# Performance work log

Measured on AMD Instinct MI355X. Metric: run time of the kernel, lower is better.

The kernel has to match this reference:

```python
import jax, jax.numpy as jnp
import numpy as np

U = 50000
I = 25000
D = 128
NUM_INTERACTIONS = 800000
NUM_LAYERS = 3


def setup_inputs() -> dict:
    key = jax.random.key(0)
    k1, k2, k3, k4 = jax.random.split(key, 4)
    # LightGCN init: nn.init.normal_(emb.weight, std=1e-4)
    user_emb = jax.random.normal(k1, (U, D), dtype=jnp.float32) * 1e-4
    item_emb = jax.random.normal(k2, (I, D), dtype=jnp.float32) * 1e-4
    # Bipartite interactions; item node ids offset by U. Symmetric adjacency.
    u = jax.random.randint(k3, (NUM_INTERACTIONS,), 0, U, dtype=jnp.int32)
    it = jax.random.randint(k4, (NUM_INTERACTIONS,), U, U + I, dtype=jnp.int32)
    edge_src = jnp.concatenate([u, it])  # [E] destination rows of adj_t
    edge_dst = jnp.concatenate([it, u])  # [E] source cols (neighbors)
    return {"user_emb": user_emb, "item_emb": item_emb,
            "edge_src": edge_src, "edge_dst": edge_dst}


def reference(user_emb, item_emb, edge_src, edge_dst):
    N = U + I
    x = jnp.concatenate([user_emb, item_emb], axis=0)  # [N, D]
    # gcn_norm without self-loops: w_ij = deg_i^-1/2 * deg_j^-1/2
    ones = jnp.ones(edge_src.shape[0], dtype=x.dtype)
    deg = jax.ops.segment_sum(ones, edge_src, num_segments=N)
    dinv = jnp.where(deg > 0, jax.lax.rsqrt(jnp.maximum(deg, 1.0)), 0.0)
    w = dinv[edge_src] * dinv[edge_dst]  # [E]
    scale = 1.0 / (NUM_LAYERS + 1)
    avg = x * scale
    for _ in range(NUM_LAYERS):
        # SpMM: out[i] = sum_{j in N(i)} w_ij * x[j]
        x = jax.ops.segment_sum(w[:, None] * x[edge_dst], edge_src, num_segments=N)
        avg = avg + x * scale
    return avg[:U], avg[U:]
```

## Files before the change

### kernel.cpp

```cpp
#include <hip/hip_runtime.h>
#include <hip/hip_fp16.h>

#define U_N 50000
#define I_N 25000
#define D_N 128
#define N_N (U_N + I_N)

#define ROWS_PER_B 256
#define NBUCK 293
#define NBLK 256
#define SN (NBUCK * NBLK)

#define SCAN_ELEMS_PER_BLOCK 1024
#define NUM_SCAN_BLOCKS ((SN + SCAN_ELEMS_PER_BLOCK - 1) / SCAN_ELEMS_PER_BLOCK)
#define SN_PAD (NUM_SCAN_BLOCKS * SCAN_ELEMS_PER_BLOCK)

typedef float f4v __attribute__((ext_vector_type(4)));
typedef float f2v __attribute__((ext_vector_type(2)));
typedef unsigned int u2v __attribute__((ext_vector_type(2)));

__global__ __launch_bounds__(256) void part_hist_kernel(const int* __restrict__ src,
                                                        int* __restrict__ hist,
                                                        int E, int chunk) {
    __shared__ int h[NBUCK];
    int t = threadIdx.x;
    for (int i = t; i < NBUCK; i += 256) h[i] = 0;
    __syncthreads();
    int b = blockIdx.x;
    int s = b * chunk;
    int e = min(E, s + chunk);
    for (int i = s + t; i < e; i += 256)
        atomicAdd(&h[src[i] >> 8], 1);
    __syncthreads();
    for (int i = t; i < NBUCK; i += 256)
        hist[i * NBLK + b] = h[i];
}

__global__ __launch_bounds__(256) void block_sums_kernel(const int4* __restrict__ cnt4,
                                                         int* __restrict__ bsums) {
    int t = threadIdx.x;
    int idx = blockIdx.x * 256 + t;
    int4 v = cnt4[idx];
    int s = v.x + v.y + v.z + v.w;
    for (int off = 32; off; off >>= 1) s += __shfl_down(s, off);
    __shared__ int wsum[4];
    int wid = t >> 6, lane = t & 63;
    if (lane == 0) wsum[wid] = s;
    __syncthreads();
    if (t == 0) bsums[blockIdx.x] = wsum[0] + wsum[1] + wsum[2] + wsum[3];
}

__global__ __launch_bounds__(128) void scan_bsums_kernel(const int* __restrict__ bsums,
                                                         int* __restrict__ boffs, int nb) {
    __shared__ int sd[128];
    int t = threadIdx.x;
    int v = (t < nb) ? bsums[t] : 0;
    sd[t] = v;
    __syncthreads();
    for (int off = 1; off < 128; off <<= 1) {
        int add = (t >= off) ? sd[t - off] : 0;
        __syncthreads();
        sd[t] += add;
        __syncthreads();
    }
    if (t < nb) boffs[t] = sd[t] - v;
}

__global__ __launch_bounds__(256) void local_scan_offs_kernel(const int4* __restrict__ cnt4,
                                                              const int* __restrict__ boffs,
                                                              int4* __restrict__ offs4) {
    int t = threadIdx.x;
    int gidx = blockIdx.x * 256 + t;
    int4 v = cnt4[gidx];
    int p0 = v.x, p1 = p0 + v.y, p2 = p1 + v.z, p3 = p2 + v.w;
    int tsum = p3;
    int lane = t & 63, wid = t >> 6;
    int incl = tsum;
    for (int off = 1; off < 64; off <<= 1) {
        int u = __shfl_up(incl, off);
        if (lane >= off) incl += u;
    }
    int lexcl = incl - tsum;
    __shared__ int wsum[4];
    if (lane == 63) wsum[wid] = incl;
    __syncthreads();
    int woff = 0;
    for (int w = 0; w < wid; ++w) woff += wsum[w];
    int base = boffs[blockIdx.x] + woff + lexcl;
    int4 o;
    o.x = base; o.y = base + p0; o.z = base + p1; o.w = base + p2;
    offs4[gidx] = o;
}

__global__ __launch_bounds__(256) void partition_kernel(const int* __restrict__ src,
                                                        const int* __restrict__ dst,
                                                        const int* __restrict__ offs,
                                                        int2* __restrict__ part,
                                                        int E, int chunk) {
    __shared__ int c[NBUCK];
    int t = threadIdx.x;
    int b = blockIdx.x;
    for (int i = t; i < NBUCK; i += 256) c[i] = offs[i * NBLK + b];
    __syncthreads();
    int s = b * chunk;
    int e = min(E, s + chunk);
    for (int i = s + t; i < e; i += 256) {
        int sv = src[i];
        int dv = dst[i];
        int pos = atomicAdd(&c[sv >> 8], 1);
        part[pos] = make_int2(sv, dv);
    }
}

__global__ __launch_bounds__(256) void bucket_csr_kernel(const int2* __restrict__ part,
                                                         const int* __restrict__ offs,
                                                         int* __restrict__ row_ptr,
                                                         float* __restrict__ dinv,
                                                         int* __restrict__ csr_dst, int E) {
    int B = blockIdx.x;
    int t = threadIdx.x;
    int bstart = offs[B * NBLK];
    int bend = (B + 1 < NBUCK) ? offs[(B + 1) * NBLK] : E;
    __shared__ int cnt_s[ROWS_PER_B];
    __shared__ int base_s[ROWS_PER_B];
    __shared__ int wsum[4];
    cnt_s[t] = 0;
    __syncthreads();
    for (int i = bstart + t; i < bend; i += 256)
        atomicAdd(&cnt_s[part[i].x & 255], 1);
    __syncthreads();
    int v = cnt_s[t];
    int lane = t & 63, wid = t >> 6;
    int incl = v;
    for (int off = 1; off < 64; off <<= 1) {
        int u = __shfl_up(incl, off);
        if (lane >= off) incl += u;
    }
    if (lane == 63) wsum[wid] = incl;
    __syncthreads();
    int woff = 0;
    for (int w = 0; w < wid; ++w) woff += wsum[w];
    int excl = woff + incl - v;
    int gid = B * ROWS_PER_B + t;
    if (gid <= N_N) row_ptr[gid] = bstart + excl;
    if (gid < N_N)  dinv[gid] = (v > 0) ? rsqrtf((float)v) : 0.0f;
    base_s[t] = bstart + excl;
    __syncthreads();
    cnt_s[t] = 0;
    __syncthreads();
    for (int i = bstart + t; i < bend; i += 256) {
        int2 ev = part[i];
        int lr = ev.x & 255;
        int pos = base_s[lr] + atomicAdd(&cnt_s[lr], 1);
        csr_dst[pos] = ev.y;
    }
}

__global__ __launch_bounds__(256) void init_kernel(const f4v* __restrict__ ue,
                                                   const f4v* __restrict__ ie,
                                                   const float* __restrict__ dinv,
                                                   __half2* __restrict__ x) {
    const int NU4 = U_N * D_N / 4;
    const int NT4 = N_N * D_N / 4;
    int i = blockIdx.x * blockDim.x + threadIdx.x;
    if (i >= NT4) return;
    f4v v = (i < NU4) ? ue[i] : ie[i - NU4];
    float di = dinv[i >> 5];
    __half2 h0 = __floats2half2_rn(di * v.x, di * v.y);
    __half2 h1 = __floats2half2_rn(di * v.z, di * v.w);
    u2v uu = { *(unsigned int*)&h0, *(unsigned int*)&h1 };
    *(u2v*)(x + 2 * (size_t)i) = uu;
}

__global__ __launch_bounds__(256) void spmm_mid_kernel(const __half2* __restrict__ x,
                                                       __half2* __restrict__ xn,
                                                       const float* __restrict__ dinv,
                                                       const int* __restrict__ row_ptr,
                                                       const int* __restrict__ csr_dst) {
    int row = (int)((blockIdx.x * blockDim.x + threadIdx.x) >> 6);
    int lane = threadIdx.x & 63;
    int beg = __builtin_amdgcn_readfirstlane(row_ptr[row]);
    int end = __builtin_amdgcn_readfirstlane(row_ptr[row + 1]);
    float di = dinv[row];
    const __half2* xc = x + lane;
    float accx = 0.0f, accy = 0.0f;
    int k = beg;
    for (; k + 16 <= end; k += 16) {
        int j[16];
        #pragma unroll
        for (int u = 0; u < 16; ++u) j[u] = csr_dst[k + u];
        #pragma unroll
        for (int u = 0; u < 16; ++u) {
            float2 f = __half22float2(xc[(size_t)j[u] * 64]);
            accx += f.x; accy += f.y;
        }
    }
    for (; k + 8 <= end; k += 8) {
        int j[8];
        #pragma unroll
        for (int u = 0; u < 8; ++u) j[u] = csr_dst[k + u];
        #pragma unroll
        for (int u = 0; u < 8; ++u) {
            float2 f = __half22float2(xc[(size_t)j[u] * 64]);
            accx += f.x; accy += f.y;
        }
    }
    for (; k < end; ++k) {
        float2 f = __half22float2(xc[(size_t)csr_dst[k] * 64]);
        accx += f.x; accy += f.y;
    }
    float s = di * di;
    __half2 h = __floats2half2_rn(s * accx, s * accy);
    *(unsigned int*)(xn + (size_t)row * 64 + lane) = __builtin_bit_cast(unsigned int, h);
}

__global__ __launch_bounds__(256) void spmm_final_kernel(const __half2* __restrict__ x2p,
                                                         const __half2* __restrict__ x1p,
                                                         const __half2* __restrict__ x0p,
                                                         const float* __restrict__ ue,
                                                         const float* __restrict__ ie,
                                                         float* __restrict__ avg,
                                                         const float* __restrict__ dinv,
                                                         const int* __restrict__ row_ptr,
                                                         const int* __restrict__ csr_dst) {
    int row = (int)((blockIdx.x * blockDim.x + threadIdx.x) >> 6);
    int lane = threadIdx.x & 63;
    int beg = __builtin_amdgcn_readfirstlane(row_ptr[row]);
    int end = __builtin_amdgcn_readfirstlane(row_ptr[row + 1]);
    float di = dinv[row];
    const __half2* xc = x2p + lane;
    float accx = 0.0f, accy = 0.0f;
    int k = beg;
    for (; k + 16 <= end; k += 16) {
        int j[16];
        #pragma unroll
        for (int u = 0; u < 16; ++u) j[u] = csr_dst[k + u];
        #pragma unroll
        for (int u = 0; u < 16; ++u) {
            float2 f = __half22float2(xc[(size_t)j[u] * 64]);
            accx += f.x; accy += f.y;
        }
    }
    for (; k + 8 <= end; k += 8) {
        int j[8];
        #pragma unroll
        for (int u = 0; u < 8; ++u) j[u] = csr_dst[k + u];
        #pragma unroll
        for (int u = 0; u < 8; ++u) {
            float2 f = __half22float2(xc[(size_t)j[u] * 64]);
            accx += f.x; accy += f.y;
        }
    }
    for (; k < end; ++k) {
        float2 f = __half22float2(xc[(size_t)csr_dst[k] * 64]);
        accx += f.x; accy += f.y;
    }
    f2v a;
    size_t ro = (size_t)row * 64 + lane;
    if (di > 0.0f) {
        float rs = 1.0f / di;
        float2 q0 = __half22float2(x0p[ro]);
        float2 q1 = __half22float2(x1p[ro]);
        float2 q2 = __half22float2(x2p[ro]);
        a.x = 0.25f * (rs * (q0.x + q1.x + q2.x) + di * accx);
        a.y = 0.25f * (rs * (q0.y + q1.y + q2.y) + di * accy);
    } else {
        const float* x0r = (row < U_N) ? (ue + (size_t)row * D_N)
                                       : (ie + (size_t)(row - U_N) * D_N);
        f2v v = *(const f2v*)(x0r + lane * 2);
        a.x = 0.25f * v.x;
        a.y = 0.25f * v.y;
    }
    __builtin_nontemporal_store(a, (f2v*)(avg + (size_t)row * D_N + lane * 2));
}

extern "C" void kernel_launch(void* const* d_in, const int* in_sizes, int n_in,
                              void* d_out, int out_size, void* d_ws, size_t ws_size,
                              hipStream_t stream) {
    const float* ue  = (const float*)d_in[0];
    const float* ie  = (const float*)d_in[1];
    const int* esrc  = (const int*)d_in[2];
    const int* edst  = (const int*)d_in[3];
    float* avg = (float*)d_out;
    const int E = in_sizes[2];
    const int N = N_N;

    char* ws = (char*)d_ws;
    size_t off = 0;
    auto alloc = [&](size_t bytes) -> void* {
        void* p = (void*)(ws + off);
        off += bytes;
        off = (off + 255) & ~((size_t)255);
        return p;
    };
    __half2* x0     = (__half2*)alloc((size_t)N * D_N * sizeof(__half));
    __half2* x1     = (__half2*)alloc((size_t)N * D_N * sizeof(__half));
    __half2* x2     = (__half2*)alloc((size_t)N * D_N * sizeof(__half));
    int*   hist     = (int*)  alloc((size_t)SN_PAD * sizeof(int));
    int*   offs     = (int*)  alloc((size_t)SN_PAD * sizeof(int));
    int*   row_ptr  = (int*)  alloc((size_t)(N + 1) * sizeof(int));
    float* dinv     = (float*)alloc((size_t)N * sizeof(float));
    int*   bsums    = (int*)  alloc((size_t)NUM_SCAN_BLOCKS * sizeof(int));
    int*   boffs    = (int*)  alloc((size_t)NUM_SCAN_BLOCKS * sizeof(int));
    int2*  part     = (int2*) alloc((size_t)E * sizeof(int2));
    int*   csr_dst  = (int*)  alloc((size_t)E * sizeof(int));

    hipMemsetAsync(hist, 0, (size_t)SN_PAD * sizeof(int), stream);
    int chunk = (E + NBLK - 1) / NBLK;
    part_hist_kernel<<<NBLK, 256, 0, stream>>>(esrc, hist, E, chunk);
    block_sums_kernel<<<NUM_SCAN_BLOCKS, 256, 0, stream>>>((const int4*)hist, bsums);
    scan_bsums_kernel<<<1, 128, 0, stream>>>(bsums, boffs, NUM_SCAN_BLOCKS);
    local_scan_offs_kernel<<<NUM_SCAN_BLOCKS, 256, 0, stream>>>((const int4*)hist, boffs,
                                                                (int4*)offs);
    partition_kernel<<<NBLK, 256, 0, stream>>>(esrc, edst, offs, part, E, chunk);
    bucket_csr_kernel<<<NBUCK, 256, 0, stream>>>(part, offs, row_ptr, dinv, csr_dst, E);

    const int NT4 = N * D_N / 4;
    init_kernel<<<(NT4 + 255) / 256, 256, 0, stream>>>(
        (const f4v*)ue, (const f4v*)ie, dinv, x0);

    int sblocks = (N * 64) / 256;
    spmm_mid_kernel<<<sblocks, 256, 0, stream>>>(x0, x1, dinv, row_ptr, csr_dst);
    spmm_mid_kernel<<<sblocks, 256, 0, stream>>>(x1, x2, dinv, row_ptr, csr_dst);
    spmm_final_kernel<<<sblocks, 256, 0, stream>>>(x2, x1, x0, ue, ie, avg, dinv,
                                                   row_ptr, csr_dst);
}
```

Before: 215.0 us.

## Fuse CSR build and init into one cooperative kernel with grid syncs

Replaces the memset and seven separate preprocessing launches (histogram, block sums, scan, offsets, partition, bucket CSR, init) with a single cooperative kernel that separates phases with grid-wide syncs. It aims to remove the launch and inter-kernel gaps of the small setup kernels. In exchange, the bucket CSR and init phases run on only 256 persistent blocks with grid-stride loops, which lowers parallelism for those phases and adds grid.sync costs.

```diff
diff --git a/kernel.cpp b/kernel.cpp
--- a/kernel.cpp
+++ b/kernel.cpp
@@ -1,5 +1,8 @@
 #include <hip/hip_runtime.h>
 #include <hip/hip_fp16.h>
+#include <hip/hip_cooperative_groups.h>
+
+namespace cg = cooperative_groups;
 
 #define U_N 50000
 #define I_N 25000
@@ -19,157 +22,148 @@
 typedef float f2v __attribute__((ext_vector_type(2)));
 typedef unsigned int u2v __attribute__((ext_vector_type(2)));
 
-__global__ __launch_bounds__(256) void part_hist_kernel(const int* __restrict__ src,
-                                                        int* __restrict__ hist,
-                                                        int E, int chunk) {
-    __shared__ int h[NBUCK];
-    int t = threadIdx.x;
-    for (int i = t; i < NBUCK; i += 256) h[i] = 0;
-    __syncthreads();
-    int b = blockIdx.x;
-    int s = b * chunk;
-    int e = min(E, s + chunk);
-    for (int i = s + t; i < e; i += 256)
-        atomicAdd(&h[src[i] >> 8], 1);
-    __syncthreads();
-    for (int i = t; i < NBUCK; i += 256)
-        hist[i * NBLK + b] = h[i];
-}
-
-__global__ __launch_bounds__(256) void block_sums_kernel(const int4* __restrict__ cnt4,
-                                                         int* __restrict__ bsums) {
-    int t = threadIdx.x;
-    int idx = blockIdx.x * 256 + t;
-    int4 v = cnt4[idx];
-    int s = v.x + v.y + v.z + v.w;
-    for (int off = 32; off; off >>= 1) s += __shfl_down(s, off);
-    __shared__ int wsum[4];
-    int wid = t >> 6, lane = t & 63;
-    if (lane == 0) wsum[wid] = s;
-    __syncthreads();
-    if (t == 0) bsums[blockIdx.x] = wsum[0] + wsum[1] + wsum[2] + wsum[3];
-}
-
-__global__ __launch_bounds__(128) void scan_bsums_kernel(const int* __restrict__ bsums,
-                                                         int* __restrict__ boffs, int nb) {
-    __shared__ int sd[128];
-    int t = threadIdx.x;
-    int v = (t < nb) ? bsums[t] : 0;
-    sd[t] = v;
-    __syncthreads();
-    for (int off = 1; off < 128; off <<= 1) {
-        int add = (t >= off) ? sd[t - off] : 0;
-        __syncthreads();
-        sd[t] += add;
-        __syncthreads();
-    }
-    if (t < nb) boffs[t] = sd[t] - v;
-}
-
-__global__ __launch_bounds__(256) void local_scan_offs_kernel(const int4* __restrict__ cnt4,
-                                                              const int* __restrict__ boffs,
-                                                              int4* __restrict__ offs4) {
-    int t = threadIdx.x;
-    int gidx = blockIdx.x * 256 + t;
-    int4 v = cnt4[gidx];
-    int p0 = v.x, p1 = p0 + v.y, p2 = p1 + v.z, p3 = p2 + v.w;
-    int tsum = p3;
-    int lane = t & 63, wid = t >> 6;
-    int incl = tsum;
-    for (int off = 1; off < 64; off <<= 1) {
-        int u = __shfl_up(incl, off);
-        if (lane >= off) incl += u;
-    }
-    int lexcl = incl - tsum;
-    __shared__ int wsum[4];
-    if (lane == 63) wsum[wid] = incl;
-    __syncthreads();
-    int woff = 0;
-    for (int w = 0; w < wid; ++w) woff += wsum[w];
-    int base = boffs[blockIdx.x] + woff + lexcl;
-    int4 o;
-    o.x = base; o.y = base + p0; o.z = base + p1; o.w = base + p2;
-    offs4[gidx] = o;
-}
-
-__global__ __launch_bounds__(256) void partition_kernel(const int* __restrict__ src,
-                                                        const int* __restrict__ dst,
-                                                        const int* __restrict__ offs,
-                                                        int2* __restrict__ part,
-                                                        int E, int chunk) {
-    __shared__ int c[NBUCK];
+__global__ __launch_bounds__(256) void build_init_kernel(
+    const int* __restrict__ esrc, const int* __restrict__ edst,
+    int* __restrict__ hist, int* __restrict__ bsums, int* __restrict__ boffs,
+    int* __restrict__ offs, int* __restrict__ row_ptr, float* __restrict__ dinv,
+    int2* __restrict__ part, int* __restrict__ csr_dst,
+    const f4v* __restrict__ ue, const f4v* __restrict__ ie,
+    __half2* __restrict__ x0, int E, int chunk)
+{
+    cg::grid_group grid = cg::this_grid();
+    __shared__ int smem[520];
     int t = threadIdx.x;
     int b = blockIdx.x;
-    for (int i = t; i < NBUCK; i += 256) c[i] = offs[i * NBLK + b];
-    __syncthreads();
-    int s = b * chunk;
-    int e = min(E, s + chunk);
-    for (int i = s + t; i < e; i += 256) {
-        int sv = src[i];
-        int dv = dst[i];
-        int pos = atomicAdd(&c[sv >> 8], 1);
-        part[pos] = make_int2(sv, dv);
-    }
-}
-
-__global__ __launch_bounds__(256) void bucket_csr_kernel(const int2* __restrict__ part,
-                                                         const int* __restrict__ offs,
-                                                         int* __restrict__ row_ptr,
-                                                         float* __restrict__ dinv,
-                                                         int* __restrict__ csr_dst, int E) {
-    int B = blockIdx.x;
-    int t = threadIdx.x;
-    int bstart = offs[B * NBLK];
-    int bend = (B + 1 < NBUCK) ? offs[(B + 1) * NBLK] : E;
-    __shared__ int cnt_s[ROWS_PER_B];
-    __shared__ int base_s[ROWS_PER_B];
-    __shared__ int wsum[4];
-    cnt_s[t] = 0;
-    __syncthreads();
-    for (int i = bstart + t; i < bend; i += 256)
-        atomicAdd(&cnt_s[part[i].x & 255], 1);
-    __syncthreads();
-    int v = cnt_s[t];
     int lane = t & 63, wid = t >> 6;
-    int incl = v;
-    for (int off = 1; off < 64; off <<= 1) {
-        int u = __shfl_up(incl, off);
-        if (lane >= off) incl += u;
-    }
-    if (lane == 63) wsum[wid] = incl;
-    __syncthreads();
-    int woff = 0;
-    for (int w = 0; w < wid; ++w) woff += wsum[w];
-    int excl = woff + incl - v;
-    int gid = B * ROWS_PER_B + t;
-    if (gid <= N_N) row_ptr[gid] = bstart + excl;
-    if (gid < N_N)  dinv[gid] = (v > 0) ? rsqrtf((float)v) : 0.0f;
-    base_s[t] = bstart + excl;
-    __syncthreads();
-    cnt_s[t] = 0;
-    __syncthreads();
-    for (int i = bstart + t; i < bend; i += 256) {
-        int2 ev = part[i];
-        int lr = ev.x & 255;
-        int pos = base_s[lr] + atomicAdd(&cnt_s[lr], 1);
-        csr_dst[pos] = ev.y;
-    }
-}
-
-__global__ __launch_bounds__(256) void init_kernel(const f4v* __restrict__ ue,
-                                                   const f4v* __restrict__ ie,
-                                                   const float* __restrict__ dinv,
-                                                   __half2* __restrict__ x) {
+
+    {
+        int* h = smem;
+        for (int i = t; i < NBUCK; i += 256) h[i] = 0;
+        __syncthreads();
+        int s = b * chunk, e = min(E, s + chunk);
+        for (int i = s + t; i < e; i += 256) atomicAdd(&h[esrc[i] >> 8], 1);
+        __syncthreads();
+        for (int i = t; i < NBUCK; i += 256) hist[i * NBLK + b] = h[i];
+        if (b == 0)
+            for (int i = SN + t; i < SN_PAD; i += 256) hist[i] = 0;
+    }
+    grid.sync();
+
+    if (b < NUM_SCAN_BLOCKS) {
+        const int4* cnt4 = (const int4*)hist;
+        int4 v = cnt4[b * 256 + t];
+        int s = v.x + v.y + v.z + v.w;
+        for (int off2 = 32; off2; off2 >>= 1) s += __shfl_down(s, off2);
+        int* wsum = smem;
+        if (lane == 0) wsum[wid] = s;
+        __syncthreads();
+        if (t == 0) bsums[b] = wsum[0] + wsum[1] + wsum[2] + wsum[3];
+    }
+    grid.sync();
+
+    if (b == 0) {
+        int* sd = smem;
+        int v = (t < NUM_SCAN_BLOCKS) ? bsums[t] : 0;
+        sd[t] = v;
+        __syncthreads();
+        for (int off2 = 1; off2 < 256; off2 <<= 1) {
+            int add = (t >= off2) ? sd[t - off2] : 0;
+            __syncthreads();
+            sd[t] += add;
+            __syncthreads();
+        }
+        if (t < NUM_SCAN_BLOCKS) boffs[t] = sd[t] - v;
+    }
+    grid.sync();
+
+    if (b < NUM_SCAN_BLOCKS) {
+        const int4* cnt4 = (const int4*)hist;
+        int gidx = b * 256 + t;
+        int4 v = cnt4[gidx];
+        int p0 = v.x, p1 = p0 + v.y, p2 = p1 + v.z, p3 = p2 + v.w;
+        int tsum = p3;
+        int incl = tsum;
+        for (int off2 = 1; off2 < 64; off2 <<= 1) {
+            int u = __shfl_up(incl, off2);
+            if (lane >= off2) incl += u;
+        }
+        int lexcl = incl - tsum;
+        int* wsum = smem;
+        if (lane == 63) wsum[wid] = incl;
+        __syncthreads();
+        int woff = 0;
+        for (int w = 0; w < wid; ++w) woff += wsum[w];
+        int base = boffs[b] + woff + lexcl;
+        int4 o;
+        o.x = base; o.y = base + p0; o.z = base + p1; o.w = base + p2;
+        ((int4*)offs)[gidx] = o;
+    }
+    grid.sync();
+
+    {
+        int* c = smem;
+        for (int i = t; i < NBUCK; i += 256) c[i] = offs[i * NBLK + b];
+        __syncthreads();
+        int s = b * chunk, e = min(E, s + chunk);
+        for (int i = s + t; i < e; i += 256) {
+            int sv = esrc[i];
+            int dv = edst[i];
+            int pos = atomicAdd(&c[sv >> 8], 1);
+            part[pos] = make_int2(sv, dv);
+        }
+    }
+    grid.sync();
+
+    for (int B = b; B < NBUCK; B += NBLK) {
+        __syncthreads();
+        int* cnt_s  = smem;
+        int* base_s = smem + 256;
+        int* wsum   = smem + 512;
+        int bstart = offs[B * NBLK];
+        int bend = (B + 1 < NBUCK) ? offs[(B + 1) * NBLK] : E;
+        cnt_s[t] = 0;
+        __syncthreads();
+        for (int i = bstart + t; i < bend; i += 256)
+            atomicAdd(&cnt_s[part[i].x & 255], 1);
+        __syncthreads();
+        int v = cnt_s[t];
+        int incl = v;
+        for (int off2 = 1; off2 < 64; off2 <<= 1) {
+            int u = __shfl_up(incl, off2);
+            if (lane >= off2) incl += u;
+        }
+        if (lane == 63) wsum[wid] = incl;
+        __syncthreads();
+        int woff = 0;
+        for (int w = 0; w < wid; ++w) woff += wsum[w];
+        int excl = woff + incl - v;
+        int gid = B * ROWS_PER_B + t;
+        if (gid <= N_N) row_ptr[gid] = bstart + excl;
+        if (gid < N_N)  dinv[gid] = (v > 0) ? rsqrtf((float)v) : 0.0f;
+        base_s[t] = bstart + excl;
+        __syncthreads();
+        cnt_s[t] = 0;
+        __syncthreads();
+        for (int i = bstart + t; i < bend; i += 256) {
+            int2 ev = part[i];
+            int lr = ev.x & 255;
+            int pos = base_s[lr] + atomicAdd(&cnt_s[lr], 1);
+            csr_dst[pos] = ev.y;
+        }
+    }
+    grid.sync();
+
     const int NU4 = U_N * D_N / 4;
     const int NT4 = N_N * D_N / 4;
-    int i = blockIdx.x * blockDim.x + threadIdx.x;
-    if (i >= NT4) return;
-    f4v v = (i < NU4) ? ue[i] : ie[i - NU4];
-    float di = dinv[i >> 5];
-    __half2 h0 = __floats2half2_rn(di * v.x, di * v.y);
-    __half2 h1 = __floats2half2_rn(di * v.z, di * v.w);
-    u2v uu = { *(unsigned int*)&h0, *(unsigned int*)&h1 };
-    *(u2v*)(x + 2 * (size_t)i) = uu;
+    for (int i = b * 256 + t; i < NT4; i += NBLK * 256) {
+        f4v v = (i < NU4) ? ue[i] : ie[i - NU4];
+        float di = dinv[i >> 5];
+        __half2 h0 = __floats2half2_rn(di * v.x, di * v.y);
+        __half2 h1 = __floats2half2_rn(di * v.z, di * v.w);
+        u2v uu = { __builtin_bit_cast(unsigned int, h0),
+                   __builtin_bit_cast(unsigned int, h1) };
+        *(u2v*)(x0 + 2 * (size_t)i) = uu;
+    }
 }
 
 __global__ __launch_bounds__(256) void spmm_mid_kernel(const __half2* __restrict__ x,
@@ -282,7 +276,7 @@
     const int* esrc  = (const int*)d_in[2];
     const int* edst  = (const int*)d_in[3];
     float* avg = (float*)d_out;
-    const int E = in_sizes[2];
+    int E = in_sizes[2];
     const int N = N_N;
 
     char* ws = (char*)d_ws;
@@ -305,19 +299,13 @@
     int2*  part     = (int2*) alloc((size_t)E * sizeof(int2));
     int*   csr_dst  = (int*)  alloc((size_t)E * sizeof(int));
 
-    hipMemsetAsync(hist, 0, (size_t)SN_PAD * sizeof(int), stream);
     int chunk = (E + NBLK - 1) / NBLK;
-    part_hist_kernel<<<NBLK, 256, 0, stream>>>(esrc, hist, E, chunk);
-    block_sums_kernel<<<NUM_SCAN_BLOCKS, 256, 0, stream>>>((const int4*)hist, bsums);
-    scan_bsums_kernel<<<1, 128, 0, stream>>>(bsums, boffs, NUM_SCAN_BLOCKS);
-    local_scan_offs_kernel<<<NUM_SCAN_BLOCKS, 256, 0, stream>>>((const int4*)hist, boffs,
-                                                                (int4*)offs);
-    partition_kernel<<<NBLK, 256, 0, stream>>>(esrc, edst, offs, part, E, chunk);
-    bucket_csr_kernel<<<NBUCK, 256, 0, stream>>>(part, offs, row_ptr, dinv, csr_dst, E);
-
-    const int NT4 = N * D_N / 4;
-    init_kernel<<<(NT4 + 255) / 256, 256, 0, stream>>>(
-        (const f4v*)ue, (const f4v*)ie, dinv, x0);
+    void* args[] = { (void*)&esrc, (void*)&edst, (void*)&hist, (void*)&bsums,
+                     (void*)&boffs, (void*)&offs, (void*)&row_ptr, (void*)&dinv,
+                     (void*)&part, (void*)&csr_dst, (void*)&ue, (void*)&ie,
+                     (void*)&x0, (void*)&E, (void*)&chunk };
+    hipLaunchCooperativeKernel((void*)build_init_kernel, dim3(NBLK), dim3(256),
+                               args, 0, stream);
 
     int sblocks = (N * 64) / 256;
     spmm_mid_kernel<<<sblocks, 256, 0, stream>>>(x0, x1, dinv, row_ptr, csr_dst);
```

Measured after the change: 407.0 us. +89.3%, slower.

## Fuse embedding init into bucket CSR build and pack partition entries

Applied to the files above, without the earlier changes.

Fuses the fp16 embedding scaling/init into the bucket CSR kernel, using a shared-memory copy of dinv so the separate init launch goes away. Packs each partition entry into one 32-bit word (local row in the top 8 bits, dst in the low 24 bits) to halve partition traffic. Doubles the partition block count to 512 and widens the block-sum scan to match. Replaces the hist memset by having block 0 zero the padding tail. In exchange, the init work now runs on only 293 blocks, and the 24-bit dst field limits node ids to below 2^24.

```diff
diff --git a/kernel.cpp b/kernel.cpp
--- a/kernel.cpp
+++ b/kernel.cpp
@@ -8,7 +8,7 @@
 
 #define ROWS_PER_B 256
 #define NBUCK 293
-#define NBLK 256
+#define NBLK 512
 #define SN (NBUCK * NBLK)
 
 #define SCAN_ELEMS_PER_BLOCK 1024
@@ -34,6 +34,8 @@
     __syncthreads();
     for (int i = t; i < NBUCK; i += 256)
         hist[i * NBLK + b] = h[i];
+    if (b == 0)
+        for (int i = SN + t; i < SN_PAD; i += 256) hist[i] = 0;
 }
 
 __global__ __launch_bounds__(256) void block_sums_kernel(const int4* __restrict__ cnt4,
@@ -50,14 +52,14 @@
     if (t == 0) bsums[blockIdx.x] = wsum[0] + wsum[1] + wsum[2] + wsum[3];
 }
 
-__global__ __launch_bounds__(128) void scan_bsums_kernel(const int* __restrict__ bsums,
+__global__ __launch_bounds__(256) void scan_bsums_kernel(const int* __restrict__ bsums,
                                                          int* __restrict__ boffs, int nb) {
-    __shared__ int sd[128];
+    __shared__ int sd[256];
     int t = threadIdx.x;
     int v = (t < nb) ? bsums[t] : 0;
     sd[t] = v;
     __syncthreads();
-    for (int off = 1; off < 128; off <<= 1) {
+    for (int off = 1; off < 256; off <<= 1) {
         int add = (t >= off) ? sd[t - off] : 0;
         __syncthreads();
         sd[t] += add;
@@ -95,7 +97,7 @@
 __global__ __launch_bounds__(256) void partition_kernel(const int* __restrict__ src,
                                                         const int* __restrict__ dst,
                                                         const int* __restrict__ offs,
-                                                        int2* __restrict__ part,
+                                                        unsigned int* __restrict__ part,
                                                         int E, int chunk) {
     __shared__ int c[NBUCK];
     int t = threadIdx.x;
@@ -108,26 +110,27 @@
         int sv = src[i];
         int dv = dst[i];
         int pos = atomicAdd(&c[sv >> 8], 1);
-        part[pos] = make_int2(sv, dv);
-    }
-}
-
-__global__ __launch_bounds__(256) void bucket_csr_kernel(const int2* __restrict__ part,
-                                                         const int* __restrict__ offs,
-                                                         int* __restrict__ row_ptr,
-                                                         float* __restrict__ dinv,
-                                                         int* __restrict__ csr_dst, int E) {
+        part[pos] = ((unsigned int)(sv & 255) << 24) | (unsigned int)dv;
+    }
+}
+
+__global__ __launch_bounds__(256) void bucket_csr_init_kernel(
+    const unsigned int* __restrict__ part, const int* __restrict__ offs,
+    int* __restrict__ row_ptr, float* __restrict__ dinv, int* __restrict__ csr_dst,
+    const f4v* __restrict__ ue, const f4v* __restrict__ ie,
+    __half2* __restrict__ x0, int E) {
     int B = blockIdx.x;
     int t = threadIdx.x;
     int bstart = offs[B * NBLK];
     int bend = (B + 1 < NBUCK) ? offs[(B + 1) * NBLK] : E;
     __shared__ int cnt_s[ROWS_PER_B];
     __shared__ int base_s[ROWS_PER_B];
+    __shared__ float dinv_s[ROWS_PER_B];
     __shared__ int wsum[4];
     cnt_s[t] = 0;
     __syncthreads();
     for (int i = bstart + t; i < bend; i += 256)
-        atomicAdd(&cnt_s[part[i].x & 255], 1);
+        atomicAdd(&cnt_s[part[i] >> 24], 1);
     __syncthreads();
     int v = cnt_s[t];
     int lane = t & 63, wid = t >> 6;
@@ -142,34 +145,34 @@
     for (int w = 0; w < wid; ++w) woff += wsum[w];
     int excl = woff + incl - v;
     int gid = B * ROWS_PER_B + t;
+    float dv = (v > 0) ? rsqrtf((float)v) : 0.0f;
     if (gid <= N_N) row_ptr[gid] = bstart + excl;
-    if (gid < N_N)  dinv[gid] = (v > 0) ? rsqrtf((float)v) : 0.0f;
+    if (gid < N_N)  dinv[gid] = dv;
+    dinv_s[t] = dv;
     base_s[t] = bstart + excl;
     __syncthreads();
     cnt_s[t] = 0;
     __syncthreads();
     for (int i = bstart + t; i < bend; i += 256) {
-        int2 ev = part[i];
-        int lr = ev.x & 255;
+        unsigned int ev = part[i];
+        int lr = ev >> 24;
         int pos = base_s[lr] + atomicAdd(&cnt_s[lr], 1);
-        csr_dst[pos] = ev.y;
-    }
-}
-
-__global__ __launch_bounds__(256) void init_kernel(const f4v* __restrict__ ue,
-                                                   const f4v* __restrict__ ie,
-                                                   const float* __restrict__ dinv,
-                                                   __half2* __restrict__ x) {
+        csr_dst[pos] = (int)(ev & 0xFFFFFFu);
+    }
     const int NU4 = U_N * D_N / 4;
     const int NT4 = N_N * D_N / 4;
-    int i = blockIdx.x * blockDim.x + threadIdx.x;
-    if (i >= NT4) return;
-    f4v v = (i < NU4) ? ue[i] : ie[i - NU4];
-    float di = dinv[i >> 5];
-    __half2 h0 = __floats2half2_rn(di * v.x, di * v.y);
-    __half2 h1 = __floats2half2_rn(di * v.z, di * v.w);
-    u2v uu = { *(unsigned int*)&h0, *(unsigned int*)&h1 };
-    *(u2v*)(x + 2 * (size_t)i) = uu;
+    int base4 = B * (ROWS_PER_B * (D_N / 4));
+    for (int i = t; i < ROWS_PER_B * (D_N / 4); i += 256) {
+        int idx = base4 + i;
+        if (idx >= NT4) break;
+        f4v val = (idx < NU4) ? ue[idx] : ie[idx - NU4];
+        float di = dinv_s[i >> 5];
+        __half2 h0 = __floats2half2_rn(di * val.x, di * val.y);
+        __half2 h1 = __floats2half2_rn(di * val.z, di * val.w);
+        u2v uu = { __builtin_bit_cast(unsigned int, h0),
+                   __builtin_bit_cast(unsigned int, h1) };
+        *(u2v*)(x0 + 2 * (size_t)idx) = uu;
+    }
 }
 
 __global__ __launch_bounds__(256) void spmm_mid_kernel(const __half2* __restrict__ x,
@@ -302,22 +305,19 @@
     float* dinv     = (float*)alloc((size_t)N * sizeof(float));
     int*   bsums    = (int*)  alloc((size_t)NUM_SCAN_BLOCKS * sizeof(int));
     int*   boffs    = (int*)  alloc((size_t)NUM_SCAN_BLOCKS * sizeof(int));
-    int2*  part     = (int2*) alloc((size_t)E * sizeof(int2));
+    unsigned int* part = (unsigned int*)alloc((size_t)E * sizeof(unsigned int));
     int*   csr_dst  = (int*)  alloc((size_t)E * sizeof(int));
 
-    hipMemsetAsync(hist, 0, (size_t)SN_PAD * sizeof(int), stream);
     int chunk = (E + NBLK - 1) / NBLK;
     part_hist_kernel<<<NBLK, 256, 0, stream>>>(esrc, hist, E, chunk);
     block_sums_kernel<<<NUM_SCAN_BLOCKS, 256, 0, stream>>>((const int4*)hist, bsums);
-    scan_bsums_kernel<<<1, 128, 0, stream>>>(bsums, boffs, NUM_SCAN_BLOCKS);
+    scan_bsums_kernel<<<1, 256, 0, stream>>>(bsums, boffs, NUM_SCAN_BLOCKS);
     local_scan_offs_kernel<<<NUM_SCAN_BLOCKS, 256, 0, stream>>>((const int4*)hist, boffs,
                                                                 (int4*)offs);
     partition_kernel<<<NBLK, 256, 0, stream>>>(esrc, edst, offs, part, E, chunk);
-    bucket_csr_kernel<<<NBUCK, 256, 0, stream>>>(part, offs, row_ptr, dinv, csr_dst, E);
-
-    const int NT4 = N * D_N / 4;
-    init_kernel<<<(NT4 + 255) / 256, 256, 0, stream>>>(
-        (const f4v*)ue, (const f4v*)ie, dinv, x0);
+    bucket_csr_init_kernel<<<NBUCK, 256, 0, stream>>>(part, offs, row_ptr, dinv, csr_dst,
+                                                      (const f4v*)ue, (const f4v*)ie,
+                                                      x0, E);
 
     int sblocks = (N * 64) / 256;
     spmm_mid_kernel<<<sblocks, 256, 0, stream>>>(x0, x1, dinv, row_ptr, csr_dst);
```

Result: faster. 209.3 us (median of 2 runs) (-2.6%).
